# Kernel tuning notes

Hardware: AMD Instinct MI355X
Metric: run time of the kernel (lower is better)

## Reference

```python
import jax, jax.numpy as jnp
import numpy as np

# SHOT descriptor hyperparameters (match init_kwargs defaults)
K_LRF = 16        # neighbors_for_lrf
A_BINS = 8        # azimuth bins
E_BINS = 2        # elevation bins
R_BINS = 2        # radial bins
H_BINS = 11       # cosine-histogram bins
EPS = 1e-8


def knn_shot_lrf(vertices, k):
    """vertices: (N,3). Returns lrfs (N,3,3) with column 0 = normal,
    neighborhoods (N,k,3) relative coords, neighbor indices (N,k)."""
    # Pairwise squared distances (N,N) -- dominant memory-bound intermediate.
    d2 = jnp.sum((vertices[:, None, :] - vertices[None, :, :]) ** 2, axis=-1)
    neg_d2, idx = jax.lax.top_k(-d2, k)                 # k nearest (incl. self)
    dists = jnp.sqrt(jnp.maximum(-neg_d2, 0.0))         # (N,k)
    neighborhoods = vertices[idx] - vertices[:, None, :]  # (N,k,3)

    # SHOT local reference frame: distance-weighted covariance + eigh.
    radius = dists[:, -1]                                # (N,) support radius
    w = jnp.maximum(radius[:, None] - dists, 0.0)        # (N,k)
    cov = jnp.einsum('nk,nki,nkj->nij', w, neighborhoods, neighborhoods)
    cov = cov / (jnp.sum(w, axis=-1)[:, None, None] + EPS)
    _, evecs = jnp.linalg.eigh(cov)                      # ascending eigenvalues
    n = evecs[..., 0]                                    # normal: smallest eval
    x = evecs[..., 2]                                    # x-axis: largest eval

    # Sign disambiguation: orient each axis with the majority of neighbors.
    proj_n = jnp.einsum('nki,ni->nk', neighborhoods, n)
    n = n * jnp.where(jnp.sum(jnp.sign(proj_n), axis=-1) >= 0, 1.0, -1.0)[:, None]
    proj_x = jnp.einsum('nki,ni->nk', neighborhoods, x)
    x = x * jnp.where(jnp.sum(jnp.sign(proj_x), axis=-1) >= 0, 1.0, -1.0)[:, None]
    y = jnp.cross(n, x)
    lrfs = jnp.stack([n, x, y], axis=-1)                 # lrfs[..., 0] = normal
    return lrfs, neighborhoods, idx


def shot_descr(neighborhoods, normals, neighborhood_indices, radius):
    """Spherical-grid (azimuth x elevation x radial) histograms of normal cosines."""
    N, k, _ = neighborhoods.shape
    nbr_normals = normals[neighborhood_indices]          # (N,k,3) irregular gather
    cos = jnp.clip(jnp.einsum('ni,nki->nk', normals, nbr_normals), -1.0, 1.0)

    r = jnp.linalg.norm(neighborhoods, axis=-1)          # (N,k)
    xg, yg, zg = neighborhoods[..., 0], neighborhoods[..., 1], neighborhoods[..., 2]

    az = jnp.arctan2(yg, xg)                                             # [-pi, pi]
    az_bin = jnp.clip(((az + jnp.pi) / (2.0 * jnp.pi) * A_BINS).astype(jnp.int32), 0, A_BINS - 1)
    el = (zg / (r + EPS) + 1.0) * 0.5                                    # [0, 1]
    el_bin = jnp.clip((el * E_BINS).astype(jnp.int32), 0, E_BINS - 1)
    rad_bin = jnp.clip((r / (radius + EPS) * R_BINS).astype(jnp.int32), 0, R_BINS - 1)
    h_bin = jnp.clip(((cos + 1.0) * 0.5 * H_BINS).astype(jnp.int32), 0, H_BINS - 1)

    flat = ((az_bin * E_BINS + el_bin) * R_BINS + rad_bin) * H_BINS + h_bin  # (N,k)
    mask = (r <= radius).astype(neighborhoods.dtype)

    total = A_BINS * E_BINS * R_BINS * H_BINS
    descr = jnp.zeros((N, total), neighborhoods.dtype)
    descr = descr.at[jnp.arange(N)[:, None], flat].add(mask)             # scatter-add
    return descr / (jnp.linalg.norm(descr, axis=-1, keepdims=True) + EPS)


def _one_cloud(vertices):
    lrfs, nbh, idx = knn_shot_lrf(vertices, K_LRF)
    # sphere_radius == 0.0 branch: global max neighborhood extent
    radius = jnp.max(jnp.linalg.norm(nbh, axis=-1))
    return shot_descr(nbh, lrfs[..., 0], idx, radius)


def setup_inputs() -> dict:
    key = jax.random.key(0)
    vertices = jax.random.normal(key, (8, 4096, 3), dtype=jnp.float32)
    return {"vertices": vertices}


def reference(vertices):
    # (B, N, 3) -> (B, N, 352)
    return jax.vmap(_one_cloud)(vertices)
```

## Files before the change

kernel.cpp:

```cpp
#include <hip/hip_runtime.h>
#include <math.h>

#define NPTS 4096
#define KNN 16
#define TBINS 352
#define PPB 16
#define CITER (NPTS / 16)
#define CAP 96
#define BINOFF 210
#define HROW 68

__device__ __forceinline__ void ins16(unsigned long long* K, unsigned long long key) {
  if (key < K[15]) {
#pragma unroll
    for (int q = 15; q >= 1; --q) {
      bool ltm = key < K[q - 1];
      bool ltk = key < K[q];
      K[q] = ltm ? K[q - 1] : (ltk ? key : K[q]);
    }
    if (key < K[0]) K[0] = key;
  }
}

#define JROT(App, Aqq, Apq, Arp, Arq, V0p, V0q, V1p, V1q, V2p, V2q)            \
  do {                                                                         \
    double apq_ = Apq;                                                         \
    if (fabs(apq_) > 1e-300) {                                                 \
      double tau_ = (Aqq - App) / (2.0 * apq_);                                \
      double t_ = (tau_ >= 0.0) ? 1.0 / (tau_ + sqrt(1.0 + tau_ * tau_))       \
                                : 1.0 / (tau_ - sqrt(1.0 + tau_ * tau_));      \
      double c_ = 1.0 / sqrt(1.0 + t_ * t_);                                   \
      double s_ = t_ * c_;                                                     \
      App = App - t_ * apq_;                                                   \
      Aqq = Aqq + t_ * apq_;                                                   \
      Apq = 0.0;                                                               \
      double u_, w_;                                                           \
      u_ = Arp; w_ = Arq; Arp = c_ * u_ - s_ * w_; Arq = s_ * u_ + c_ * w_;    \
      u_ = V0p; w_ = V0q; V0p = c_ * u_ - s_ * w_; V0q = s_ * u_ + c_ * w_;    \
      u_ = V1p; w_ = V1q; V1p = c_ * u_ - s_ * w_; V1q = s_ * u_ + c_ * w_;    \
      u_ = V2p; w_ = V2q; V2p = c_ * u_ - s_ * w_; V2q = s_ * u_ + c_ * w_;    \
    }                                                                          \
  } while (0)

__global__ __launch_bounds__(256, 4) void knn_hist_kernel(
    const float* __restrict__ verts,
    float* __restrict__ normals,
    int* __restrict__ nbr_idx,
    unsigned int* __restrict__ radius_bits)
{
  __shared__ unsigned char hist[256 * HROW];
  __shared__ unsigned short ptot[PPB][64];
  __shared__ unsigned long long surv[PPB][CAP];
  __shared__ unsigned int scnt[PPB];
  __shared__ unsigned int tbl[PPB];

  const int blk = blockIdx.x;
  const int cloud = blk >> 8;
  const int pbase = (blk & 255) * PPB;
  const float* __restrict__ vb = verts + (size_t)cloud * NPTS * 3;
  const int tid = (int)threadIdx.x;

  {
    unsigned int* h32 = (unsigned int*)hist;
#pragma unroll
    for (int k = 0; k < 17; ++k) h32[tid * 17 + k] = 0u;
  }
  if (tid < PPB) scnt[tid] = 0u;
  __syncthreads();

  const int p = tid >> 4;
  const int c = tid & 15;
  const int i = pbase + p;
  const float xi = vb[3 * i + 0], yi = vb[3 * i + 1], zi = vb[3 * i + 2];

#pragma unroll 4
  for (int s = 0; s < CITER; ++s) {
    const int j = (s << 4) | c;
    const float* vp = vb + 3 * j;
    float dx = __fsub_rn(vp[0], xi);
    float dy = __fsub_rn(vp[1], yi);
    float dz = __fsub_rn(vp[2], zi);
    float d2 = __fadd_rn(__fadd_rn(__fmul_rn(dx, dx), __fmul_rn(dy, dy)),
                         __fmul_rn(dz, dz));
    int b = (int)(__float_as_uint(d2) >> 22) - BINOFF;
    b = min(max(b, 0), 63);
    hist[tid * HROW + b] += (unsigned char)1;
  }
  __syncthreads();

#pragma unroll
  for (int bq = 0; bq < 4; ++bq) {
    int b = 4 * c + bq;
    unsigned int tot = 0;
    for (int r = 0; r < 16; ++r) tot += hist[(p * 16 + r) * HROW + b];
    ptot[p][b] = (unsigned short)tot;
  }
  __syncthreads();

  if (c == 0) {
    unsigned int cum = 0; int B = 63;
    for (int b = 0; b < 64; ++b) {
      cum += ptot[p][b];
      if (cum >= KNN) { B = b; break; }
    }
    tbl[p] = (B >= 63) ? 0xFFFFFFFFu : ((unsigned int)(B + 1 + BINOFF) << 22);
  }
  __syncthreads();

  {
    const unsigned int T = tbl[p];
#pragma unroll 4
    for (int s = 0; s < CITER; ++s) {
      const int j = (s << 4) | c;
      const float* vp = vb + 3 * j;
      float dx = __fsub_rn(vp[0], xi);
      float dy = __fsub_rn(vp[1], yi);
      float dz = __fsub_rn(vp[2], zi);
      float d2 = __fadd_rn(__fadd_rn(__fmul_rn(dx, dx), __fmul_rn(dy, dy)),
                           __fmul_rn(dz, dz));
      unsigned int bits = __float_as_uint(d2);
      if (bits < T) {
        unsigned int pos = atomicAdd(&scnt[p], 1u);
        if (pos < CAP) surv[p][pos] = ((unsigned long long)bits << 32) | (unsigned int)j;
      }
    }
  }
  __syncthreads();

  if (c != 0) return;

  unsigned long long K[KNN];
#pragma unroll
  for (int k = 0; k < KNN; ++k) K[k] = 0xFFFFFFFFFFFFFFFFull;
  const int n = (int)scnt[p];
  if (n <= CAP) {
    for (int t = 0; t < n; ++t) ins16(K, surv[p][t]);
  } else {
    for (int j = 0; j < NPTS; ++j) {
      const float* vp = vb + 3 * j;
      float dx = __fsub_rn(vp[0], xi);
      float dy = __fsub_rn(vp[1], yi);
      float dz = __fsub_rn(vp[2], zi);
      float d2 = __fadd_rn(__fadd_rn(__fmul_rn(dx, dx), __fmul_rn(dy, dy)),
                           __fmul_rn(dz, dz));
      ins16(K, ((unsigned long long)__float_as_uint(d2) << 32) | (unsigned int)j);
    }
  }

  float v[KNN]; int id[KNN];
#pragma unroll
  for (int k = 0; k < KNN; ++k) {
    v[k] = __uint_as_float((unsigned int)(K[k] >> 32));
    id[k] = (int)(K[k] & 0xFFFFFFFFull);
  }

  double dist[KNN];
#pragma unroll
  for (int k = 0; k < KNN; ++k) dist[k] = sqrt((double)v[k]);
  const double radius_i = dist[KNN - 1];

  float ddx[KNN], ddy[KNN], ddz[KNN];
  double c00 = 0, c01 = 0, c02 = 0, c11 = 0, c12 = 0, c22 = 0, sw = 0;
#pragma unroll
  for (int k = 0; k < KNN; ++k) {
    const float* vp = vb + 3 * id[k];
    float dx = __fsub_rn(vp[0], xi);
    float dy = __fsub_rn(vp[1], yi);
    float dz = __fsub_rn(vp[2], zi);
    ddx[k] = dx; ddy[k] = dy; ddz[k] = dz;
    double w = radius_i - dist[k];
    if (w < 0.0) w = 0.0;
    double dxd = dx, dyd = dy, dzd = dz;
    double wx = w * dxd, wy = w * dyd;
    c00 = fma(wx, dxd, c00);
    c01 = fma(wx, dyd, c01);
    c02 = fma(wx, dzd, c02);
    c11 = fma(wy, dyd, c11);
    c12 = fma(wy, dzd, c12);
    c22 = fma(w * dzd, dzd, c22);
    sw += w;
  }
  double inv = 1.0 / (sw + 1e-8);
  c00 *= inv; c01 *= inv; c02 *= inv; c11 *= inv; c12 *= inv; c22 *= inv;

  double A00 = c00, A01 = c01, A02 = c02, A11 = c11, A12 = c12, A22 = c22;
  double v00 = 1, v01 = 0, v02 = 0,
         v10 = 0, v11 = 1, v12 = 0,
         v20 = 0, v21 = 0, v22 = 1;
  for (int sweep = 0; sweep < 8; ++sweep) {
    JROT(A00, A11, A01, A02, A12, v00, v01, v10, v11, v20, v21);
    JROT(A00, A22, A02, A01, A12, v00, v02, v10, v12, v20, v22);
    JROT(A11, A22, A12, A01, A02, v01, v02, v11, v12, v21, v22);
  }

  double nx, ny, nz;
  if (A00 <= A11 && A00 <= A22)      { nx = v00; ny = v10; nz = v20; }
  else if (A11 <= A22)               { nx = v01; ny = v11; nz = v21; }
  else                               { nx = v02; ny = v12; nz = v22; }
  double rn = 1.0 / sqrt(nx * nx + ny * ny + nz * nz);
  nx *= rn; ny *= rn; nz *= rn;

  int sv = 0;
#pragma unroll
  for (int k = 0; k < KNN; ++k) {
    double pr = (double)ddx[k] * nx + (double)ddy[k] * ny + (double)ddz[k] * nz;
    sv += (pr > 0.0) - (pr < 0.0);
  }
  if (sv < 0) { nx = -nx; ny = -ny; nz = -nz; }

  const int gp = cloud * NPTS + i;
  normals[3 * gp + 0] = (float)nx;
  normals[3 * gp + 1] = (float)ny;
  normals[3 * gp + 2] = (float)nz;
#pragma unroll
  for (int k = 0; k < KNN; ++k) nbr_idx[gp * KNN + k] = id[k];

  atomicMax(&radius_bits[cloud], __float_as_uint((float)radius_i));
}

__global__ __launch_bounds__(256) void bins_kernel(
    const float* __restrict__ verts,
    const float* __restrict__ normals,
    const int* __restrict__ nbr_idx,
    const unsigned int* __restrict__ radius_bits,
    unsigned short* __restrict__ bins,
    float* __restrict__ denoms)
{
  const int gp = blockIdx.x * 256 + threadIdx.x;
  const int cloud = gp >> 12;
  const int i = gp & (NPTS - 1);
  const float* __restrict__ vb = verts + (size_t)cloud * NPTS * 3;
  const float xi = vb[3 * i + 0], yi = vb[3 * i + 1], zi = vb[3 * i + 2];
  const float nxi = normals[3 * gp + 0];
  const float nyi = normals[3 * gp + 1];
  const float nzi = normals[3 * gp + 2];
  const float radius = __uint_as_float(radius_bits[cloud]);
  const float rpe = __fadd_rn(radius, 1e-8f);
  const float PI_F = 3.14159274101257324f;
  const float TWOPI_F = 6.28318548202514648f;

  int bl[KNN];
#pragma unroll
  for (int k = 0; k < KNN; ++k) {
    int j = nbr_idx[gp * KNN + k];
    float dx = __fsub_rn(vb[3 * j + 0], xi);
    float dy = __fsub_rn(vb[3 * j + 1], yi);
    float dz = __fsub_rn(vb[3 * j + 2], zi);
    float d2f = __fadd_rn(__fadd_rn(__fmul_rn(dx, dx), __fmul_rn(dy, dy)),
                          __fmul_rn(dz, dz));
    float r = (float)sqrt((double)d2f);

    float az = (float)atan2((double)dy, (double)dx);
    int azb = (int)__fmul_rn(__fdiv_rn(__fadd_rn(az, PI_F), TWOPI_F), 8.0f);
    azb = min(max(azb, 0), 7);

    float el = __fmul_rn(__fadd_rn(__fdiv_rn(dz, __fadd_rn(r, 1e-8f)), 1.0f), 0.5f);
    int elb = (int)__fmul_rn(el, 2.0f);
    elb = min(max(elb, 0), 1);

    int rb = (int)__fmul_rn(__fdiv_rn(r, rpe), 2.0f);
    rb = min(max(rb, 0), 1);

    int gj = cloud * NPTS + j;
    double cd = (double)nxi * (double)normals[3 * gj + 0] +
                (double)nyi * (double)normals[3 * gj + 1] +
                (double)nzi * (double)normals[3 * gj + 2];
    cd = fmin(fmax(cd, -1.0), 1.0);
    float cf = (float)cd;
    int hb = (int)__fmul_rn(__fmul_rn(__fadd_rn(cf, 1.0f), 0.5f), 11.0f);
    hb = min(max(hb, 0), 10);

    bl[k] = ((azb * 2 + elb) * 2 + rb) * 11 + hb;
  }

  int pairs = 0;
#pragma unroll
  for (int a = 0; a < KNN; ++a)
#pragma unroll
    for (int b = 0; b < KNN; ++b) pairs += (bl[a] == bl[b]) ? 1 : 0;

  denoms[gp] = __fadd_rn(sqrtf((float)pairs), 1e-8f);
  unsigned short* bp = bins + (size_t)gp * KNN;
#pragma unroll
  for (int k = 0; k < KNN; ++k) bp[k] = (unsigned short)bl[k];
}

__global__ __launch_bounds__(256) void out_kernel(
    const unsigned short* __restrict__ bins,
    const float* __restrict__ denoms,
    float* __restrict__ out)
{
  const int gid = blockIdx.x * 256 + threadIdx.x;
  const int p = gid / TBINS;
  const int b = gid - p * TBINS;
  const unsigned short* __restrict__ bp = bins + (size_t)p * KNN;
  int c = 0;
#pragma unroll
  for (int k = 0; k < KNN; ++k) c += (bp[k] == (unsigned short)b) ? 1 : 0;
  out[gid] = __fdiv_rn((float)c, denoms[p]);
}

extern "C" void kernel_launch(void* const* d_in, const int* in_sizes, int n_in,
                              void* d_out, int out_size, void* d_ws, size_t ws_size,
                              hipStream_t stream) {
  const float* verts = (const float*)d_in[0];
  float* out = (float*)d_out;

  char* ws = (char*)d_ws;
  float* normals = (float*)ws;
  int* nidx = (int*)(ws + 393216);
  unsigned short* bins = (unsigned short*)(ws + 2490368);
  float* denoms = (float*)(ws + 3538944);
  unsigned int* radb = (unsigned int*)(ws + 3670016);

  hipMemsetAsync(radb, 0, 8 * sizeof(unsigned int), stream);

  knn_hist_kernel<<<2048, 256, 0, stream>>>(verts, normals, nidx, radb);
  bins_kernel<<<128, 256, 0, stream>>>(verts, normals, nidx, radb, bins, denoms);
  const int total = 8 * NPTS * TBINS;
  out_kernel<<<total / 256, 256, 0, stream>>>(bins, denoms, out);
}
```

Measured before the change: 344.6 us.

## Split kNN selection and LRF normal computation into separate kernels

Moves the double-precision covariance, Jacobi eigen-solve and sign disambiguation out of the kNN selection kernel into a new normal_kernel launched with 64-thread blocks. The selection kernel now only writes neighbor indices, and its launch bounds change from 4 to 2 blocks per multiprocessor. Distances are recomputed from the gathered neighbors. The aim is to lower register pressure in the heavy selection kernel and run the eigen-solve at its own occupancy, at the cost of an extra launch and a round trip through global memory for the indices.

```diff
diff --git a/kernel.cpp b/kernel.cpp
--- a/kernel.cpp
+++ b/kernel.cpp
@@ -42,11 +42,9 @@
     }                                                                          \
   } while (0)
 
-__global__ __launch_bounds__(256, 4) void knn_hist_kernel(
+__global__ __launch_bounds__(256, 2) void knn_select_kernel(
     const float* __restrict__ verts,
-    float* __restrict__ normals,
-    int* __restrict__ nbr_idx,
-    unsigned int* __restrict__ radius_bits)
+    int* __restrict__ nbr_idx)
 {
   __shared__ unsigned char hist[256 * HROW];
   __shared__ unsigned short ptot[PPB][64];
@@ -147,20 +145,29 @@
     }
   }
 
-  float v[KNN]; int id[KNN];
-#pragma unroll
-  for (int k = 0; k < KNN; ++k) {
-    v[k] = __uint_as_float((unsigned int)(K[k] >> 32));
-    id[k] = (int)(K[k] & 0xFFFFFFFFull);
-  }
-
+  const int gp = cloud * NPTS + i;
+#pragma unroll
+  for (int k = 0; k < KNN; ++k) nbr_idx[gp * KNN + k] = (int)(K[k] & 0xFFFFFFFFull);
+}
+
+__global__ void normal_kernel(
+    const float* __restrict__ verts,
+    const int* __restrict__ nbr_idx,
+    float* __restrict__ normals,
+    unsigned int* __restrict__ radius_bits)
+{
+  const int gp = blockIdx.x * 64 + (int)threadIdx.x;
+  const int cloud = gp >> 12;
+  const int i = gp & (NPTS - 1);
+  const float* __restrict__ vb = verts + (size_t)cloud * NPTS * 3;
+  const float xi = vb[3 * i + 0], yi = vb[3 * i + 1], zi = vb[3 * i + 2];
+
+  int id[KNN];
+#pragma unroll
+  for (int k = 0; k < KNN; ++k) id[k] = nbr_idx[gp * KNN + k];
+
+  float ddx[KNN], ddy[KNN], ddz[KNN];
   double dist[KNN];
-#pragma unroll
-  for (int k = 0; k < KNN; ++k) dist[k] = sqrt((double)v[k]);
-  const double radius_i = dist[KNN - 1];
-
-  float ddx[KNN], ddy[KNN], ddz[KNN];
-  double c00 = 0, c01 = 0, c02 = 0, c11 = 0, c12 = 0, c22 = 0, sw = 0;
 #pragma unroll
   for (int k = 0; k < KNN; ++k) {
     const float* vp = vb + 3 * id[k];
@@ -168,9 +175,18 @@
     float dy = __fsub_rn(vp[1], yi);
     float dz = __fsub_rn(vp[2], zi);
     ddx[k] = dx; ddy[k] = dy; ddz[k] = dz;
+    float d2 = __fadd_rn(__fadd_rn(__fmul_rn(dx, dx), __fmul_rn(dy, dy)),
+                         __fmul_rn(dz, dz));
+    dist[k] = sqrt((double)d2);
+  }
+  const double radius_i = dist[KNN - 1];
+
+  double c00 = 0, c01 = 0, c02 = 0, c11 = 0, c12 = 0, c22 = 0, sw = 0;
+#pragma unroll
+  for (int k = 0; k < KNN; ++k) {
     double w = radius_i - dist[k];
     if (w < 0.0) w = 0.0;
-    double dxd = dx, dyd = dy, dzd = dz;
+    double dxd = ddx[k], dyd = ddy[k], dzd = ddz[k];
     double wx = w * dxd, wy = w * dyd;
     c00 = fma(wx, dxd, c00);
     c01 = fma(wx, dyd, c01);
@@ -208,12 +224,9 @@
   }
   if (sv < 0) { nx = -nx; ny = -ny; nz = -nz; }
 
-  const int gp = cloud * NPTS + i;
   normals[3 * gp + 0] = (float)nx;
   normals[3 * gp + 1] = (float)ny;
   normals[3 * gp + 2] = (float)nz;
-#pragma unroll
-  for (int k = 0; k < KNN; ++k) nbr_idx[gp * KNN + k] = id[k];
 
   atomicMax(&radius_bits[cloud], __float_as_uint((float)radius_i));
 }
@@ -315,7 +328,8 @@
 
   hipMemsetAsync(radb, 0, 8 * sizeof(unsigned int), stream);
 
-  knn_hist_kernel<<<2048, 256, 0, stream>>>(verts, normals, nidx, radb);
+  knn_select_kernel<<<2048, 256, 0, stream>>>(verts, nidx);
+  normal_kernel<<<512, 64, 0, stream>>>(verts, nidx, normals, radb);
   bins_kernel<<<128, 256, 0, stream>>>(verts, normals, nidx, radb, bins, denoms);
   const int total = 8 * NPTS * TBINS;
   out_kernel<<<total / 256, 256, 0, stream>>>(bins, denoms, out);
```

After: 672.7 us. 1.95x slower.
